# Kernel optimization log

Hardware: AMD Instinct MI355X
Metric: run time of the kernel (lower is better)

The kernel has to match this reference:

```python
import jax, jax.numpy as jnp
import numpy as np

N = 100000
E = 1200000
C = 64
R = C // 8  # channel-attention reduced dim
G = 256    # number of graphs
EPS = 1e-5


def setup_inputs() -> dict:
    key = jax.random.key(0)
    ks = jax.random.split(key, 12)
    x = jax.random.normal(ks[0], (N, C), dtype=jnp.float32)
    edge_index = jax.random.randint(ks[1], (2, E), 0, N, dtype=jnp.int64)
    batch = jnp.sort(jax.random.randint(ks[2], (N,), 0, G, dtype=jnp.int64))
    s = 1.0 / np.sqrt(C)
    # SAGEConv: lin_l (applied to aggregated neighbors, with bias), lin_r (applied to self, no bias)
    Wl = jax.random.uniform(ks[3], (C, C), jnp.float32, -s, s)
    bl = jax.random.uniform(ks[4], (C,), jnp.float32, -s, s)
    Wr = jax.random.uniform(ks[5], (C, C), jnp.float32, -s, s)
    # GraphNorm params
    gn_w = jnp.ones((C,), jnp.float32)
    gn_b = jnp.zeros((C,), jnp.float32)
    gn_alpha = jnp.ones((C,), jnp.float32)  # mean_scale
    # ChannelAttention params
    sr = 1.0 / np.sqrt(C)
    a1_w = jax.random.uniform(ks[6], (R, C), jnp.float32, -sr, sr)
    a1_b = jax.random.uniform(ks[7], (R,), jnp.float32, -sr, sr)
    s2 = 1.0 / np.sqrt(R)
    a2_w = jax.random.uniform(ks[8], (C, R), jnp.float32, -s2, s2)
    a2_b = jax.random.uniform(ks[9], (C,), jnp.float32, -s2, s2)
    return {"x": x, "edge_index": edge_index, "batch": batch,
            "Wl": Wl, "bl": bl, "Wr": Wr,
            "gn_w": gn_w, "gn_b": gn_b, "gn_alpha": gn_alpha,
            "a1_w": a1_w, "a1_b": a1_b, "a2_w": a2_w, "a2_b": a2_b}


def _sage_conv(x, edge_index, Wl, bl, Wr):
    src, dst = edge_index[0], edge_index[1]
    # mean aggregation of neighbor features at destination nodes
    msg = x[src]  # [E, C]
    agg = jax.ops.segment_sum(msg, dst, num_segments=N)  # [N, C]
    deg = jax.ops.segment_sum(jnp.ones((E,), x.dtype), dst, num_segments=N)
    agg = agg / jnp.maximum(deg, 1.0)[:, None]
    return agg @ Wl.T + bl + x @ Wr.T


def _graph_norm(h, batch, w, b, alpha):
    cnt = jax.ops.segment_sum(jnp.ones((N,), h.dtype), batch, num_segments=G)
    cnt = jnp.maximum(cnt, 1.0)[:, None]  # [G,1]
    mean = jax.ops.segment_sum(h, batch, num_segments=G) / cnt  # [G,C]
    out = h - mean[batch] * alpha
    var = jax.ops.segment_sum(out * out, batch, num_segments=G) / cnt
    return w * out * jax.lax.rsqrt(var[batch] + EPS) + b


def reference(x, edge_index, batch, Wl, bl, Wr, gn_w, gn_b, gn_alpha,
              a1_w, a1_b, a2_w, a2_b):
    tmp = _graph_norm(_sage_conv(x, edge_index, Wl, bl, Wr), batch,
                      gn_w, gn_b, gn_alpha)
    # channel attention gate on the residual branch
    gate = jax.nn.sigmoid(jax.nn.relu(x @ a1_w.T + a1_b) @ a2_w.T + a2_b)
    tmp = tmp + gate * x
    # activation; dropout is identity at eval
    return jax.nn.relu(tmp)
```

## Files before the change

kernel.cpp:

```cpp
#include <hip/hip_runtime.h>
#include <math.h>

#define NN 100000
#define NE 1200000
#define CC 64
#define GG 256
#define RR 8
#define EPSF 1e-5f
#define BINS 782
#define BINP 1024
#define EPB 4688
#define QS 1028

__device__ inline unsigned short f2bf(float f) {
  unsigned u = __float_as_uint(f);
  return (unsigned short)((u + 0x7fffu + ((u >> 16) & 1u)) >> 16);
}
__device__ inline float bf2f(unsigned short s) {
  return __uint_as_float(((unsigned)s) << 16);
}

__global__ __launch_bounds__(256) void k_cvt(const float* __restrict__ x,
                                             unsigned short* __restrict__ xb) {
  int i = blockIdx.x * 256 + threadIdx.x;
  if (i >= NN * CC / 8) return;
  const float4* xp = (const float4*)(x + (size_t)i * 8);
  float4 a = xp[0], b = xp[1];
  uint4 o;
  o.x = (unsigned)f2bf(a.x) | ((unsigned)f2bf(a.y) << 16);
  o.y = (unsigned)f2bf(a.z) | ((unsigned)f2bf(a.w) << 16);
  o.z = (unsigned)f2bf(b.x) | ((unsigned)f2bf(b.y) << 16);
  o.w = (unsigned)f2bf(b.z) | ((unsigned)f2bf(b.w) << 16);
  *(uint4*)(xb + (size_t)i * 8) = o;
}

__global__ __launch_bounds__(256) void k_hist(const int* __restrict__ ei,
                                              int* __restrict__ bin_total) {
  __shared__ int hist[BINP];
  for (int t = threadIdx.x; t < BINP; t += 256) hist[t] = 0;
  __syncthreads();
  int start = blockIdx.x * EPB;
  int end = start + EPB < NE ? start + EPB : NE;
  for (int e = start + threadIdx.x; e < end; e += 256)
    atomicAdd(&hist[ei[NE + e] >> 7], 1);
  __syncthreads();
  for (int t = threadIdx.x; t < BINP; t += 256)
    if (hist[t]) atomicAdd(&bin_total[t], hist[t]);
}

__global__ __launch_bounds__(1024) void k_scanbins(const int* __restrict__ bin_total,
                                                   int* __restrict__ bin_base,
                                                   int* __restrict__ cursor,
                                                   int* __restrict__ rowptr) {
  __shared__ int sh[BINP];
  int t = threadIdx.x;
  int v = t < BINS ? bin_total[t] : 0;
  sh[t] = v;
  __syncthreads();
  for (int d = 1; d < BINP; d <<= 1) {
    int val = sh[t];
    int add = (t >= d) ? sh[t - d] : 0;
    __syncthreads();
    sh[t] = val + add;
    __syncthreads();
  }
  int excl = sh[t] - v;
  if (t < BINS) {
    bin_base[t] = excl;
    cursor[t] = excl;
  }
  if (t == 0) {
    bin_base[BINS] = NE;
    rowptr[NN] = NE;
  }
}

__global__ __launch_bounds__(256) void k_phase1(const int* __restrict__ ei,
                                                int* __restrict__ cursor,
                                                unsigned* __restrict__ ebuf) {
  __shared__ int hist[BINP];
  __shared__ int base[BINP];
  for (int t = threadIdx.x; t < BINP; t += 256) hist[t] = 0;
  __syncthreads();
  int start = blockIdx.x * EPB;
  int end = start + EPB < NE ? start + EPB : NE;
  for (int e = start + threadIdx.x; e < end; e += 256)
    atomicAdd(&hist[ei[NE + e] >> 7], 1);
  __syncthreads();
  for (int t = threadIdx.x; t < BINP; t += 256) {
    int c = hist[t];
    base[t] = c ? atomicAdd(&cursor[t], c) : 0;
  }
  __syncthreads();
  for (int t = threadIdx.x; t < BINP; t += 256) hist[t] = 0;
  __syncthreads();
  for (int e = start + threadIdx.x; e < end; e += 256) {
    int src = ei[e], dst = ei[NE + e];
    int b = dst >> 7;
    int off = atomicAdd(&hist[b], 1);
    ebuf[base[b] + off] = ((unsigned)src << 7) | (unsigned)(dst & 127);
  }
}

__global__ __launch_bounds__(256) void k_fill2(const unsigned* __restrict__ ebuf,
                                               const int* __restrict__ bin_base,
                                               int* __restrict__ rowptr,
                                               int* __restrict__ csr) {
  __shared__ int cnt[128];
  __shared__ int sc[128];
  int tid = threadIdx.x;
  int b = blockIdx.x;
  int s = bin_base[b], e = bin_base[b + 1];
  if (tid < 128) cnt[tid] = 0;
  __syncthreads();
  for (int i = s + tid; i < e; i += 256) atomicAdd(&cnt[ebuf[i] & 127], 1);
  __syncthreads();
  if (tid < 128) sc[tid] = cnt[tid];
  __syncthreads();
  for (int d = 1; d < 128; d <<= 1) {
    int v = (tid < 128) ? sc[tid] : 0;
    int a = (tid >= d && tid < 128) ? sc[tid - d] : 0;
    __syncthreads();
    if (tid < 128) sc[tid] = v + a;
    __syncthreads();
  }
  if (tid < 128) {
    sc[tid] -= cnt[tid];
    int node = (b << 7) + tid;
    if (node < NN) rowptr[node] = s + sc[tid];
    cnt[tid] = 0;
  }
  __syncthreads();
  for (int i = s + tid; i < e; i += 256) {
    unsigned v = ebuf[i];
    int dl = v & 127;
    int off = atomicAdd(&cnt[dl], 1);
    csr[s + sc[dl] + off] = (int)(v >> 7);
  }
}

__global__ __launch_bounds__(256) void k_gather(const unsigned short* __restrict__ xb,
                                                const int* __restrict__ csr,
                                                const int* __restrict__ rowptr,
                                                float* __restrict__ h) {
  int w = blockIdx.x * 4 + (threadIdx.x >> 6);
  int lane = threadIdx.x & 63;
  if (w >= NN) return;
  int s = rowptr[w], e = rowptr[w + 1];
  float acc = 0.0f;
  for (int j0 = s; j0 < e; j0 += 8) {
    int idx[8];
#pragma unroll
    for (int u = 0; u < 8; ++u) {
      int j = j0 + u;
      idx[u] = csr[j < e ? j : e - 1];
    }
    float v[8];
#pragma unroll
    for (int u = 0; u < 8; ++u) v[u] = bf2f(xb[(size_t)idx[u] * CC + lane]);
#pragma unroll
    for (int u = 0; u < 8; ++u) acc += (j0 + u < e) ? v[u] : 0.0f;
  }
  h[(size_t)w * CC + lane] = acc;
}

__global__ __launch_bounds__(256) void k_passA(
    const float* __restrict__ x, float* h, const int* __restrict__ rowptr,
    const float* __restrict__ Wl, const float* __restrict__ bl,
    const float* __restrict__ Wr) {
  __shared__ float WLs[4 * QS];
  __shared__ float WRs[4 * QS];
  __shared__ float bls[CC];
  for (int idx = threadIdx.x; idx < CC * CC; idx += 256) {
    int c = idx >> 6, k = idx & 63;
    int qq = c >> 4, j = c & 15;
    WLs[qq * QS + j * 64 + k] = Wl[idx];
    WRs[qq * QS + j * 64 + k] = Wr[idx];
  }
  if (threadIdx.x < CC) bls[threadIdx.x] = bl[threadIdx.x];
  __syncthreads();

  int lane = threadIdx.x & 63;
  int wave = threadIdx.x >> 6;
  int n = lane & 15;
  int q = lane >> 4;
  int i0 = blockIdx.x * 128 + wave * 32 + n;
  const float4* wl = (const float4*)(WLs + q * QS);
  const float4* wr = (const float4*)(WRs + q * QS);

  const float4* ap[2];
  const float4* xp[2];
  float inv[2];
#pragma unroll
  for (int m = 0; m < 2; ++m) {
    int i = i0 + m * 16;
    int c = i < NN ? i : NN - 1;
    inv[m] = 1.0f / fmaxf((float)(rowptr[c + 1] - rowptr[c]), 1.0f);
    ap[m] = (const float4*)(h + (size_t)c * CC);
    xp[m] = (const float4*)(x + (size_t)c * CC);
  }

  float acc[2][16];
#pragma unroll
  for (int j = 0; j < 16; ++j) {
    float b = bls[q * 16 + j];
    acc[0][j] = b; acc[1][j] = b;
  }

  for (int kbl = 0; kbl < 4; ++kbl) {
    float4 A[2][4];
#pragma unroll
    for (int m = 0; m < 2; ++m) {
#pragma unroll
      for (int t = 0; t < 4; ++t) {
        float4 v = ap[m][kbl * 4 + t];
        A[m][t] = make_float4(v.x * inv[m], v.y * inv[m], v.z * inv[m], v.w * inv[m]);
      }
    }
#pragma unroll
    for (int t = 0; t < 4; ++t) {
#pragma unroll
      for (int j = 0; j < 16; ++j) {
        float4 w = wl[j * 16 + kbl * 4 + t];
#pragma unroll
        for (int m = 0; m < 2; ++m) {
          float v = acc[m][j];
          v = fmaf(A[m][t].x, w.x, v);
          v = fmaf(A[m][t].y, w.y, v);
          v = fmaf(A[m][t].z, w.z, v);
          v = fmaf(A[m][t].w, w.w, v);
          acc[m][j] = v;
        }
      }
    }
  }

  for (int kbl = 0; kbl < 4; ++kbl) {
    float4 A[2][4];
#pragma unroll
    for (int m = 0; m < 2; ++m) {
#pragma unroll
      for (int t = 0; t < 4; ++t) A[m][t] = xp[m][kbl * 4 + t];
    }
#pragma unroll
    for (int t = 0; t < 4; ++t) {
#pragma unroll
      for (int j = 0; j < 16; ++j) {
        float4 w = wr[j * 16 + kbl * 4 + t];
#pragma unroll
        for (int m = 0; m < 2; ++m) {
          float v = acc[m][j];
          v = fmaf(A[m][t].x, w.x, v);
          v = fmaf(A[m][t].y, w.y, v);
          v = fmaf(A[m][t].z, w.z, v);
          v = fmaf(A[m][t].w, w.w, v);
          acc[m][j] = v;
        }
      }
    }
  }

#pragma unroll
  for (int m = 0; m < 2; ++m) {
    int i = i0 + m * 16;
    if (i < NN) {
      float4* hp = (float4*)(h + (size_t)i * CC + q * 16);
#pragma unroll
      for (int r = 0; r < 4; ++r)
        hp[r] = make_float4(acc[m][4 * r], acc[m][4 * r + 1],
                            acc[m][4 * r + 2], acc[m][4 * r + 3]);
    }
  }
}

__global__ __launch_bounds__(256) void k_stats(const float* __restrict__ h,
                                               const int* __restrict__ batch,
                                               float* __restrict__ sumH,
                                               float* __restrict__ sumH2,
                                               float* __restrict__ cntg) {
  int w = blockIdx.x * 4 + (threadIdx.x >> 6);
  int lane = threadIdx.x & 63;
  int i0 = w * 16;
  if (i0 >= NN) return;
  int iend = i0 + 16 < NN ? i0 + 16 : NN;
  int gcur = batch[i0];
  float aH = 0.0f, aH2 = 0.0f;
  int run = 0;
  for (int i = i0; i < iend; ++i) {
    int g = batch[i];
    if (g != gcur) {
      atomicAdd(&sumH[(size_t)gcur * CC + lane], aH);
      atomicAdd(&sumH2[(size_t)gcur * CC + lane], aH2);
      if (lane == 0) atomicAdd(&cntg[gcur], (float)run);
      aH = 0.0f; aH2 = 0.0f; run = 0;
      gcur = g;
    }
    float v = h[(size_t)i * CC + lane];
    aH += v;
    aH2 += v * v;
    run++;
  }
  atomicAdd(&sumH[(size_t)gcur * CC + lane], aH);
  atomicAdd(&sumH2[(size_t)gcur * CC + lane], aH2);
  if (lane == 0) atomicAdd(&cntg[gcur], (float)run);
}

__global__ __launch_bounds__(256) void k_passC(
    const float* __restrict__ h, const float* __restrict__ x,
    const int* __restrict__ batch, const float* __restrict__ sumH,
    const float* __restrict__ sumH2, const float* __restrict__ cntg,
    const float* __restrict__ gw, const float* __restrict__ gb,
    const float* __restrict__ alpha, const float* __restrict__ a1w,
    const float* __restrict__ a1b, const float* __restrict__ a2w,
    const float* __restrict__ a2b, float* __restrict__ out) {
  __shared__ float A1[RR * CC];
  __shared__ float A2[CC * RR];
  __shared__ float A1B[RR];
  __shared__ float PRM[4 * CC];
  for (int idx = threadIdx.x; idx < RR * CC; idx += 256) {
    A1[idx] = a1w[idx];
    A2[idx] = a2w[idx];
  }
  if (threadIdx.x < RR) A1B[threadIdx.x] = a1b[threadIdx.x];
  if (threadIdx.x < CC) {
    PRM[threadIdx.x] = a2b[threadIdx.x];
    PRM[CC + threadIdx.x] = gw[threadIdx.x];
    PRM[2 * CC + threadIdx.x] = gb[threadIdx.x];
    PRM[3 * CC + threadIdx.x] = alpha[threadIdx.x];
  }
  __syncthreads();

  int i = blockIdx.x * 256 + threadIdx.x;
  if (i >= NN) return;
  int g = batch[i];
  float rn = 1.0f / fmaxf(cntg[g], 1.0f);
  float xv[CC];
  const float4* xp = (const float4*)(x + (size_t)i * CC);
#pragma unroll
  for (int q = 0; q < 16; ++q) {
    float4 b = xp[q];
    xv[4 * q] = b.x; xv[4 * q + 1] = b.y; xv[4 * q + 2] = b.z; xv[4 * q + 3] = b.w;
  }
  float p[RR];
#pragma unroll
  for (int r = 0; r < RR; ++r) {
    float acc = A1B[r];
#pragma unroll
    for (int k = 0; k < CC; ++k) acc = fmaf(xv[k], A1[r * CC + k], acc);
    p[r] = fmaxf(acc, 0.0f);
  }
  const float4* hp = (const float4*)(h + (size_t)i * CC);
  const float4* sHp = (const float4*)(sumH + (size_t)g * CC);
  const float4* sH2p = (const float4*)(sumH2 + (size_t)g * CC);
  float4* op = (float4*)(out + (size_t)i * CC);
#pragma unroll 4
  for (int q = 0; q < 16; ++q) {
    float4 h4 = hp[q];
    float4 sH = sHp[q];
    float4 sH2 = sH2p[q];
    float hv[4] = {h4.x, h4.y, h4.z, h4.w};
    float sh[4] = {sH.x, sH.y, sH.z, sH.w};
    float sh2[4] = {sH2.x, sH2.y, sH2.z, sH2.w};
    float res[4];
#pragma unroll
    for (int u = 0; u < 4; ++u) {
      int c = q * 4 + u;
      float mu = sh[u] * rn;
      float t = PRM[3 * CC + c] * mu;
      float var = sh2[u] * rn - 2.0f * mu * t + t * t;
      float o = hv[u] - t;
      float y = fmaf(PRM[CC + c] * o, rsqrtf(var + EPSF), PRM[2 * CC + c]);
      float gacc = PRM[c];
#pragma unroll
      for (int r = 0; r < RR; ++r) gacc = fmaf(p[r], A2[c * RR + r], gacc);
      float gate = 1.0f / (1.0f + __expf(-gacc));
      res[u] = fmaxf(y + gate * xv[c], 0.0f);
    }
    op[q] = make_float4(res[0], res[1], res[2], res[3]);
  }
}

extern "C" void kernel_launch(void* const* d_in, const int* in_sizes, int n_in,
                              void* d_out, int out_size, void* d_ws, size_t ws_size,
                              hipStream_t stream) {
  const float* x        = (const float*)d_in[0];
  const int*   ei       = (const int*)d_in[1];
  const int*   batch    = (const int*)d_in[2];
  const float* Wl       = (const float*)d_in[3];
  const float* bl       = (const float*)d_in[4];
  const float* Wr       = (const float*)d_in[5];
  const float* gn_w     = (const float*)d_in[6];
  const float* gn_b     = (const float*)d_in[7];
  const float* gn_alpha = (const float*)d_in[8];
  const float* a1w      = (const float*)d_in[9];
  const float* a1b      = (const float*)d_in[10];
  const float* a2w      = (const float*)d_in[11];
  const float* a2b      = (const float*)d_in[12];
  float* out = (float*)d_out;

  float*    h        = (float*)d_ws;
  unsigned* ebuf     = (unsigned*)(h + (size_t)NN * CC);
  int*      csr      = (int*)(ebuf + NE);
  int*      rowptr   = csr + NE;
  int*      bin_tot  = rowptr + NN + 1;
  float*    sumH     = (float*)(bin_tot + BINP);
  float*    sumH2    = sumH + GG * CC;
  float*    cntg     = sumH2 + GG * CC;
  int*      bin_base = (int*)(cntg + GG);
  int*      cursor   = bin_base + BINS + 1;
  unsigned short* xb = (unsigned short*)d_out;

  size_t zbytes = ((size_t)BINP + 2 * GG * CC + GG) * sizeof(int);
  hipMemsetAsync((void*)bin_tot, 0, zbytes, stream);

  k_cvt     <<<(NN * CC / 8 + 255) / 256, 256, 0, stream>>>(x, xb);
  k_hist    <<<256, 256, 0, stream>>>(ei, bin_tot);
  k_scanbins<<<1, BINP, 0, stream>>>(bin_tot, bin_base, cursor, rowptr);
  k_phase1  <<<256, 256, 0, stream>>>(ei, cursor, ebuf);
  k_fill2   <<<BINS, 256, 0, stream>>>(ebuf, bin_base, rowptr, csr);
  k_gather  <<<(NN + 3) / 4, 256, 0, stream>>>(xb, csr, rowptr, h);
  k_passA   <<<(NN + 127) / 128, 256, 0, stream>>>(x, h, rowptr, Wl, bl, Wr);
  k_stats   <<<((NN + 15) / 16 + 3) / 4, 256, 0, stream>>>(h, batch, sumH, sumH2, cntg);
  k_passC   <<<(NN + 255) / 256, 256, 0, stream>>>(h, x, batch, sumH, sumH2, cntg,
                                                   gn_w, gn_b, gn_alpha,
                                                   a1w, a1b, a2w, a2b, out);
}
```

Measured before the change: 215.4 us.

## Compute SAGE linear layers with bf16 MFMA and store mean aggregate in bf16

The FP32 FMA matmul in passA, which used LDS-staged weights, is replaced with bf16 MFMA 16x16x32 instructions. Weights are converted to bf16 by a new small kernel, and x reuses the existing bf16 copy. The gather kernel now applies the mean normalisation itself and writes the aggregate as bf16, which halves the intermediate traffic and removes the degree lookup from passA. The cost is lower precision on the x and Wr path, and the bf16 aggregate buffer is placed in the output buffer right after xb.

```diff
diff --git a/kernel.cpp b/kernel.cpp
--- a/kernel.cpp
+++ b/kernel.cpp
@@ -10,7 +10,9 @@
 #define BINS 782
 #define BINP 1024
 #define EPB 4688
-#define QS 1028
+
+typedef __attribute__((ext_vector_type(8))) short bf16x8;
+typedef __attribute__((ext_vector_type(4))) float f32x4;
 
 __device__ inline unsigned short f2bf(float f) {
   unsigned u = __float_as_uint(f);
@@ -34,6 +36,17 @@
   *(uint4*)(xb + (size_t)i * 8) = o;
 }
 
+__global__ __launch_bounds__(256) void k_cvtW(const float* __restrict__ Wl,
+                                              const float* __restrict__ Wr,
+                                              unsigned short* __restrict__ wbl,
+                                              unsigned short* __restrict__ wbr) {
+  int i = blockIdx.x * 256 + threadIdx.x;
+  if (i < CC * CC) {
+    wbl[i] = f2bf(Wl[i]);
+    wbr[i] = f2bf(Wr[i]);
+  }
+}
+
 __global__ __launch_bounds__(256) void k_hist(const int* __restrict__ ei,
                                               int* __restrict__ bin_total) {
   __shared__ int hist[BINP];
@@ -142,7 +155,7 @@
 __global__ __launch_bounds__(256) void k_gather(const unsigned short* __restrict__ xb,
                                                 const int* __restrict__ csr,
                                                 const int* __restrict__ rowptr,
-                                                float* __restrict__ h) {
+                                                unsigned short* __restrict__ aggb) {
   int w = blockIdx.x * 4 + (threadIdx.x >> 6);
   int lane = threadIdx.x & 63;
   if (w >= NN) return;
@@ -161,114 +174,62 @@
 #pragma unroll
     for (int u = 0; u < 8; ++u) acc += (j0 + u < e) ? v[u] : 0.0f;
   }
-  h[(size_t)w * CC + lane] = acc;
+  float inv = 1.0f / fmaxf((float)(e - s), 1.0f);
+  aggb[(size_t)w * CC + lane] = f2bf(acc * inv);
 }
 
 __global__ __launch_bounds__(256) void k_passA(
-    const float* __restrict__ x, float* h, const int* __restrict__ rowptr,
-    const float* __restrict__ Wl, const float* __restrict__ bl,
-    const float* __restrict__ Wr) {
-  __shared__ float WLs[4 * QS];
-  __shared__ float WRs[4 * QS];
-  __shared__ float bls[CC];
-  for (int idx = threadIdx.x; idx < CC * CC; idx += 256) {
-    int c = idx >> 6, k = idx & 63;
-    int qq = c >> 4, j = c & 15;
-    WLs[qq * QS + j * 64 + k] = Wl[idx];
-    WRs[qq * QS + j * 64 + k] = Wr[idx];
-  }
-  if (threadIdx.x < CC) bls[threadIdx.x] = bl[threadIdx.x];
-  __syncthreads();
-
+    const unsigned short* __restrict__ xb, const unsigned short* __restrict__ aggb,
+    const unsigned short* __restrict__ wbl, const unsigned short* __restrict__ wbr,
+    const float* __restrict__ bl, float* __restrict__ h) {
   int lane = threadIdx.x & 63;
   int wave = threadIdx.x >> 6;
-  int n = lane & 15;
-  int q = lane >> 4;
-  int i0 = blockIdx.x * 128 + wave * 32 + n;
-  const float4* wl = (const float4*)(WLs + q * QS);
-  const float4* wr = (const float4*)(WRs + q * QS);
-
-  const float4* ap[2];
-  const float4* xp[2];
-  float inv[2];
-#pragma unroll
-  for (int m = 0; m < 2; ++m) {
-    int i = i0 + m * 16;
-    int c = i < NN ? i : NN - 1;
-    inv[m] = 1.0f / fmaxf((float)(rowptr[c + 1] - rowptr[c]), 1.0f);
-    ap[m] = (const float4*)(h + (size_t)c * CC);
-    xp[m] = (const float4*)(x + (size_t)c * CC);
-  }
-
-  float acc[2][16];
-#pragma unroll
-  for (int j = 0; j < 16; ++j) {
-    float b = bls[q * 16 + j];
-    acc[0][j] = b; acc[1][j] = b;
-  }
-
-  for (int kbl = 0; kbl < 4; ++kbl) {
-    float4 A[2][4];
-#pragma unroll
-    for (int m = 0; m < 2; ++m) {
-#pragma unroll
-      for (int t = 0; t < 4; ++t) {
-        float4 v = ap[m][kbl * 4 + t];
-        A[m][t] = make_float4(v.x * inv[m], v.y * inv[m], v.z * inv[m], v.w * inv[m]);
-      }
-    }
-#pragma unroll
-    for (int t = 0; t < 4; ++t) {
-#pragma unroll
-      for (int j = 0; j < 16; ++j) {
-        float4 w = wl[j * 16 + kbl * 4 + t];
-#pragma unroll
-        for (int m = 0; m < 2; ++m) {
-          float v = acc[m][j];
-          v = fmaf(A[m][t].x, w.x, v);
-          v = fmaf(A[m][t].y, w.y, v);
-          v = fmaf(A[m][t].z, w.z, v);
-          v = fmaf(A[m][t].w, w.w, v);
-          acc[m][j] = v;
-        }
-      }
-    }
-  }
-
-  for (int kbl = 0; kbl < 4; ++kbl) {
-    float4 A[2][4];
-#pragma unroll
-    for (int m = 0; m < 2; ++m) {
-#pragma unroll
-      for (int t = 0; t < 4; ++t) A[m][t] = xp[m][kbl * 4 + t];
-    }
-#pragma unroll
-    for (int t = 0; t < 4; ++t) {
-#pragma unroll
-      for (int j = 0; j < 16; ++j) {
-        float4 w = wr[j * 16 + kbl * 4 + t];
-#pragma unroll
-        for (int m = 0; m < 2; ++m) {
-          float v = acc[m][j];
-          v = fmaf(A[m][t].x, w.x, v);
-          v = fmaf(A[m][t].y, w.y, v);
-          v = fmaf(A[m][t].z, w.z, v);
-          v = fmaf(A[m][t].w, w.w, v);
-          acc[m][j] = v;
-        }
-      }
-    }
-  }
-
-#pragma unroll
-  for (int m = 0; m < 2; ++m) {
-    int i = i0 + m * 16;
-    if (i < NN) {
-      float4* hp = (float4*)(h + (size_t)i * CC + q * 16);
-#pragma unroll
-      for (int r = 0; r < 4; ++r)
-        hp[r] = make_float4(acc[m][4 * r], acc[m][4 * r + 1],
-                            acc[m][4 * r + 2], acc[m][4 * r + 3]);
+  int node0 = blockIdx.x * 64 + wave * 16;
+  if (node0 >= NN) return;
+  int lr = lane & 15;
+  int kg = lane >> 4;
+
+  bf16x8 WL[4][2], WR[4][2];
+#pragma unroll
+  for (int i = 0; i < 4; ++i)
+#pragma unroll
+    for (int t = 0; t < 2; ++t) {
+      size_t off = (size_t)(i * 16 + lr) * CC + t * 32 + kg * 8;
+      WL[i][t] = *(const bf16x8*)(wbl + off);
+      WR[i][t] = *(const bf16x8*)(wbr + off);
+    }
+
+  int arow = node0 + lr;
+  if (arow >= NN) arow = NN - 1;
+  bf16x8 Aa[2], Ax[2];
+#pragma unroll
+  for (int t = 0; t < 2; ++t) {
+    Aa[t] = *(const bf16x8*)(aggb + (size_t)arow * CC + t * 32 + kg * 8);
+    Ax[t] = *(const bf16x8*)(xb + (size_t)arow * CC + t * 32 + kg * 8);
+  }
+
+  f32x4 acc[4];
+#pragma unroll
+  for (int i = 0; i < 4; ++i) {
+    float b = bl[i * 16 + lr];
+    acc[i] = (f32x4){b, b, b, b};
+  }
+#pragma unroll
+  for (int i = 0; i < 4; ++i) {
+#pragma unroll
+    for (int t = 0; t < 2; ++t) {
+      acc[i] = __builtin_amdgcn_mfma_f32_16x16x32_bf16(Aa[t], WL[i][t], acc[i], 0, 0, 0);
+      acc[i] = __builtin_amdgcn_mfma_f32_16x16x32_bf16(Ax[t], WR[i][t], acc[i], 0, 0, 0);
+    }
+  }
+
+#pragma unroll
+  for (int r = 0; r < 4; ++r) {
+    int node = node0 + kg * 4 + r;
+    if (node < NN) {
+#pragma unroll
+      for (int i = 0; i < 4; ++i)
+        h[(size_t)node * CC + i * 16 + lr] = acc[i][r];
     }
   }
 }
@@ -408,18 +369,22 @@
   float*    cntg     = sumH2 + GG * CC;
   int*      bin_base = (int*)(cntg + GG);
   int*      cursor   = bin_base + BINS + 1;
-  unsigned short* xb = (unsigned short*)d_out;
+  unsigned short* wbl = (unsigned short*)(cursor + BINS);
+  unsigned short* wbr = wbl + CC * CC;
+  unsigned short* xb   = (unsigned short*)d_out;
+  unsigned short* aggb = xb + (size_t)NN * CC;
 
   size_t zbytes = ((size_t)BINP + 2 * GG * CC + GG) * sizeof(int);
   hipMemsetAsync((void*)bin_tot, 0, zbytes, stream);
 
   k_cvt     <<<(NN * CC / 8 + 255) / 256, 256, 0, stream>>>(x, xb);
+  k_cvtW    <<<(CC * CC + 255) / 256, 256, 0, stream>>>(Wl, Wr, wbl, wbr);
   k_hist    <<<256, 256, 0, stream>>>(ei, bin_tot);
   k_scanbins<<<1, BINP, 0, stream>>>(bin_tot, bin_base, cursor, rowptr);
   k_phase1  <<<256, 256, 0, stream>>>(ei, cursor, ebuf);
   k_fill2   <<<BINS, 256, 0, stream>>>(ebuf, bin_base, rowptr, csr);
-  k_gather  <<<(NN + 3) / 4, 256, 0, stream>>>(xb, csr, rowptr, h);
-  k_passA   <<<(NN + 127) / 128, 256, 0, stream>>>(x, h, rowptr, Wl, bl, Wr);
+  k_gather  <<<(NN + 3) / 4, 256, 0, stream>>>(xb, csr, rowptr, aggb);
+  k_passA   <<<(NN + 63) / 64, 256, 0, stream>>>(xb, aggb, wbl, wbr, bl, h);
   k_stats   <<<((NN + 15) / 16 + 3) / 4, 256, 0, stream>>>(h, batch, sumH, sumH2, cntg);
   k_passC   <<<(NN + 255) / 256, 256, 0, stream>>>(h, x, batch, sumH, sumH2, cntg,
                                                    gn_w, gn_b, gn_alpha,
```

After: 183.2 us. -14.9%, faster.
